# Kernel tuning notes

Hardware: AMD Instinct MI355X
Metric: run time of the kernel (lower is better)

Reference implementation:

```python
import jax, jax.numpy as jnp
import numpy as np

N, K, D_IN, D_OUT = 20000, 32, 128, 128


def _xavier(key, shape, gain):
    fan_out, fan_in = shape
    bound = gain * np.sqrt(6.0 / (fan_in + fan_out))
    return jax.random.uniform(key, shape, jnp.float32, -bound, bound)


def setup_inputs() -> dict:
    key = jax.random.key(0)
    ks = jax.random.split(key, 8)
    gain = np.sqrt(2.0)  # calculate_gain('relu')
    return {
        "data_x": jax.random.normal(ks[0], (N, D_IN), jnp.float32),
        "dists_max": jax.random.uniform(ks[1], (N, K), jnp.float32),
        "dists_argmax": jax.random.randint(ks[2], (N, K), 0, N, jnp.int64),
        # dist_compute: Nonlinear(1, D_OUT, 1)
        "w1d": _xavier(ks[3], (D_OUT, 1), gain),
        "b1d": jnp.zeros((D_OUT,), jnp.float32),
        "w2d": _xavier(ks[4], (1, D_OUT), gain),
        "b2d": jnp.zeros((1,), jnp.float32),
        # linear_hidden: (2*D_IN) -> D_OUT
        "wh": _xavier(ks[5], (D_OUT, 2 * D_IN), gain),
        "bh": jnp.zeros((D_OUT,), jnp.float32),
        # linear_out_position: D_OUT -> 1
        "wp": _xavier(ks[6], (1, D_OUT), gain),
        "bp": jnp.zeros((1,), jnp.float32),
    }


def reference(data_x, dists_max, dists_argmax, w1d, b1d, w2d, b2d, wh, bh, wp, bp):
    # trainable distance transform: [N,K] -> [N,K,1] -> MLP -> [N,K]
    d = jax.nn.relu(dists_max[..., None] * w1d[:, 0] + b1d)  # [N,K,D_OUT]
    d = (d @ w2d[0] + b2d[0])  # [N,K]
    # gather anchor features: [N,K,D_IN]
    subset = data_x[dists_argmax]
    messages = subset * d[..., None]
    self_feat = jnp.broadcast_to(data_x[:, None, :], messages.shape)
    cat = jnp.concatenate((messages, self_feat), axis=-1)  # [N,K,2*D_IN]
    h = jax.nn.relu(jnp.einsum('nkd,od->nko', cat, wh) + bh)  # [N,K,D_OUT]
    out_position = (h @ wp[0] + bp[0])  # [N,K]
    out_structure = jnp.mean(h, axis=1)  # [N,D_OUT]
    return out_position, out_structure
```

## Files before the change

kernel.cpp:

```cpp
#include <hip/hip_runtime.h>
#include <hip/hip_bf16.h>

#define N_ROWS 20000
#define KNN 32
#define DIN 128
#define DOUT 128

__global__ __launch_bounds__(256) void pack_wt(const float* __restrict__ wh,
                                               float* __restrict__ WTp) {
    int tid = blockIdx.x * 256 + threadIdx.x;
    int i  = tid & 3;
    int j  = (tid >> 2) & 255;
    int d4 = tid >> 10;
    int d  = d4 * 4 + i;
    float v = (j < 128) ? wh[j * 256 + d] : wh[(j - 128) * 256 + 128 + d];
    WTp[tid] = v;
}

__global__ __launch_bounds__(256) void gemm_xaxb(const float* __restrict__ x,
                                                 const float* __restrict__ WTp,
                                                 const float* __restrict__ bh,
                                                 __hip_bfloat16* __restrict__ XA16,
                                                 float* __restrict__ XBp) {
    __shared__ float xs[32][128];
    const int t = threadIdx.x;
    const int row0 = blockIdx.x * 32;

    #pragma unroll
    for (int i = 0; i < 4; ++i) {
        int idx = t + i * 256;
        int r = idx >> 5, c4 = idx & 31;
        ((float4*)xs[r])[c4] = ((const float4*)(x + (size_t)(row0 + r) * DIN))[c4];
    }
    __syncthreads();

    const int tx = t & 63;
    const int ty = t >> 6;
    const int r0 = ty * 8;
    float acc[8][4];
    #pragma unroll
    for (int r = 0; r < 8; ++r)
        #pragma unroll
        for (int c = 0; c < 4; ++c) acc[r][c] = 0.f;

    const float4* W4 = (const float4*)WTp;
    for (int d4 = 0; d4 < 32; ++d4) {
        float4 w0 = W4[d4 * 256 + tx];
        float4 w1 = W4[d4 * 256 + 64 + tx];
        float4 w2 = W4[d4 * 256 + 128 + tx];
        float4 w3 = W4[d4 * 256 + 192 + tx];
        #pragma unroll
        for (int r = 0; r < 8; ++r) {
            float4 xv = ((const float4*)xs[r0 + r])[d4];
            acc[r][0] += xv.x * w0.x + xv.y * w0.y + xv.z * w0.z + xv.w * w0.w;
            acc[r][1] += xv.x * w1.x + xv.y * w1.y + xv.z * w1.z + xv.w * w1.w;
            acc[r][2] += xv.x * w2.x + xv.y * w2.y + xv.z * w2.z + xv.w * w2.w;
            acc[r][3] += xv.x * w3.x + xv.y * w3.y + xv.z * w3.z + xv.w * w3.w;
        }
    }

    float bh0 = bh[tx], bh1 = bh[64 + tx];
    #pragma unroll
    for (int r = 0; r < 8; ++r) {
        size_t gr = row0 + r0 + r;
        XA16[gr * DOUT + tx]       = __float2bfloat16(acc[r][0]);
        XA16[gr * DOUT + 64 + tx]  = __float2bfloat16(acc[r][1]);
        XBp [gr * DOUT + tx]       = acc[r][2] + bh0;
        XBp [gr * DOUT + 64 + tx]  = acc[r][3] + bh1;
    }
}

__global__ __launch_bounds__(128) void fused_main(const float* __restrict__ dists,
                                                  const int*  __restrict__ argm,
                                                  const float* __restrict__ w1d,
                                                  const float* __restrict__ b1d,
                                                  const float* __restrict__ w2d,
                                                  const float* __restrict__ b2d,
                                                  const float* __restrict__ wp,
                                                  const float* __restrict__ bp,
                                                  const __hip_bfloat16* __restrict__ XA16,
                                                  const float* __restrict__ XBp,
                                                  float* __restrict__ out_pos,
                                                  float* __restrict__ out_struct) {
    const int w    = threadIdx.x >> 6;
    const int lane = threadIdx.x & 63;
    const int n    = blockIdx.x * 2 + w;

    __shared__ float pos_lds[2][KNN][65];
    __shared__ float d_lds[2][KNN];
    __shared__ int   idx_lds[2][KNN];

    {
        int k = lane >> 1, sub = lane & 1;
        float s = dists[(size_t)n * KNN + k];
        float a = 0.f;
        int ob = sub * 64;
        #pragma unroll
        for (int o4 = 0; o4 < 16; ++o4) {
            float4 w1 = ((const float4*)(w1d + ob))[o4];
            float4 b1 = ((const float4*)(b1d + ob))[o4];
            float4 w2 = ((const float4*)(w2d + ob))[o4];
            a += fmaxf(fmaf(s, w1.x, b1.x), 0.f) * w2.x;
            a += fmaxf(fmaf(s, w1.y, b1.y), 0.f) * w2.y;
            a += fmaxf(fmaf(s, w1.z, b1.z), 0.f) * w2.z;
            a += fmaxf(fmaf(s, w1.w, b1.w), 0.f) * w2.w;
        }
        a += __shfl_xor(a, 1);
        if (sub == 0) d_lds[w][k] = a + b2d[0];
        if (lane < KNN) idx_lds[w][lane] = argm[(size_t)n * KNN + lane];
    }

    float2 base = *(const float2*)(XBp + (size_t)n * DOUT + lane * 2);
    float2 wpv  = *(const float2*)(wp + lane * 2);
    __syncthreads();

    const unsigned short* xa_base = (const unsigned short*)XA16;
    float s0 = 0.f, s1 = 0.f;
    #pragma unroll
    for (int kk = 0; kk < KNN; ++kk) {
        float dk = d_lds[w][kk];
        int   m  = idx_lds[w][kk];
        unsigned u = *(const unsigned*)(xa_base + (size_t)m * DOUT + lane * 2);
        float xa0 = __uint_as_float(u << 16);
        float xa1 = __uint_as_float(u & 0xFFFF0000u);
        float h0 = fmaxf(fmaf(dk, xa0, base.x), 0.f);
        float h1 = fmaxf(fmaf(dk, xa1, base.y), 0.f);
        s0 += h0; s1 += h1;
        pos_lds[w][kk][lane] = fmaf(h1, wpv.y, h0 * wpv.x);
    }
    *(float2*)(out_struct + (size_t)n * DOUT + lane * 2) =
        make_float2(s0 * (1.f / KNN), s1 * (1.f / KNN));
    __syncthreads();

    {
        int k2 = lane & 31, half = lane >> 5;
        const float* row = &pos_lds[w][k2][half * 32];
        float p = 0.f;
        #pragma unroll
        for (int j = 0; j < 32; ++j) p += row[j];
        p += __shfl_xor(p, 32);
        if (lane < KNN)
            out_pos[(size_t)n * KNN + lane] = p + bp[0];
    }
}

extern "C" void kernel_launch(void* const* d_in, const int* in_sizes, int n_in,
                              void* d_out, int out_size, void* d_ws, size_t ws_size,
                              hipStream_t stream) {
    const float* data_x = (const float*)d_in[0];
    const float* dists  = (const float*)d_in[1];
    const int*   argm   = (const int*)d_in[2];
    const float* w1d    = (const float*)d_in[3];
    const float* b1d    = (const float*)d_in[4];
    const float* w2d    = (const float*)d_in[5];
    const float* b2d    = (const float*)d_in[6];
    const float* wh     = (const float*)d_in[7];
    const float* bh     = (const float*)d_in[8];
    const float* wp     = (const float*)d_in[9];
    const float* bp     = (const float*)d_in[10];

    float* out_pos    = (float*)d_out;
    float* out_struct = out_pos + (size_t)N_ROWS * KNN;

    float*          XBp  = (float*)d_ws;
    __hip_bfloat16* XA16 = (__hip_bfloat16*)(XBp + (size_t)N_ROWS * DOUT);
    float*          WTp  = (float*)((char*)XA16 + (size_t)N_ROWS * DOUT * 2);

    pack_wt<<<128, 256, 0, stream>>>(wh, WTp);
    gemm_xaxb<<<N_ROWS / 32, 256, 0, stream>>>(data_x, WTp, bh, XA16, XBp);
    fused_main<<<N_ROWS / 2, 128, 0, stream>>>(dists, argm, w1d, b1d, w2d, b2d,
                                               wp, bp, XA16, XBp, out_pos, out_struct);
}
```

Baseline: 170.5 us.

## Use one wave per row with readlane broadcasts and shuffle reductions

The fused kernel now runs one 64-thread wave per output row. The per-neighbour distance weights and indices stay in registers and are broadcast with readlane instead of being staged in LDS. The position dot product is partly reduced with lane shuffles, so only an 8-way partial sum per neighbour is written to a small LDS buffer instead of a full 32x65 array. Separately, the GEMM tile is halved to 16 rows per block to launch more blocks, at the cost of reusing each weight load across fewer rows.

After: 209.3 us. 1.23x slower.

```diff
diff --git a/kernel.cpp b/kernel.cpp
--- a/kernel.cpp
+++ b/kernel.cpp
@@ -22,12 +22,12 @@
                                                  const float* __restrict__ bh,
                                                  __hip_bfloat16* __restrict__ XA16,
                                                  float* __restrict__ XBp) {
-    __shared__ float xs[32][128];
+    __shared__ float xs[16][128];
     const int t = threadIdx.x;
-    const int row0 = blockIdx.x * 32;
+    const int row0 = blockIdx.x * 16;
 
     #pragma unroll
-    for (int i = 0; i < 4; ++i) {
+    for (int i = 0; i < 2; ++i) {
         int idx = t + i * 256;
         int r = idx >> 5, c4 = idx & 31;
         ((float4*)xs[r])[c4] = ((const float4*)(x + (size_t)(row0 + r) * DIN))[c4];
@@ -36,10 +36,10 @@
 
     const int tx = t & 63;
     const int ty = t >> 6;
-    const int r0 = ty * 8;
-    float acc[8][4];
+    const int r0 = ty * 4;
+    float acc[4][4];
     #pragma unroll
-    for (int r = 0; r < 8; ++r)
+    for (int r = 0; r < 4; ++r)
         #pragma unroll
         for (int c = 0; c < 4; ++c) acc[r][c] = 0.f;
 
@@ -50,7 +50,7 @@
         float4 w2 = W4[d4 * 256 + 128 + tx];
         float4 w3 = W4[d4 * 256 + 192 + tx];
         #pragma unroll
-        for (int r = 0; r < 8; ++r) {
+        for (int r = 0; r < 4; ++r) {
             float4 xv = ((const float4*)xs[r0 + r])[d4];
             acc[r][0] += xv.x * w0.x + xv.y * w0.y + xv.z * w0.z + xv.w * w0.w;
             acc[r][1] += xv.x * w1.x + xv.y * w1.y + xv.z * w1.z + xv.w * w1.w;
@@ -61,7 +61,7 @@
 
     float bh0 = bh[tx], bh1 = bh[64 + tx];
     #pragma unroll
-    for (int r = 0; r < 8; ++r) {
+    for (int r = 0; r < 4; ++r) {
         size_t gr = row0 + r0 + r;
         XA16[gr * DOUT + tx]       = __float2bfloat16(acc[r][0]);
         XA16[gr * DOUT + 64 + tx]  = __float2bfloat16(acc[r][1]);
@@ -70,77 +70,73 @@
     }
 }
 
-__global__ __launch_bounds__(128) void fused_main(const float* __restrict__ dists,
-                                                  const int*  __restrict__ argm,
-                                                  const float* __restrict__ w1d,
-                                                  const float* __restrict__ b1d,
-                                                  const float* __restrict__ w2d,
-                                                  const float* __restrict__ b2d,
-                                                  const float* __restrict__ wp,
-                                                  const float* __restrict__ bp,
-                                                  const __hip_bfloat16* __restrict__ XA16,
-                                                  const float* __restrict__ XBp,
-                                                  float* __restrict__ out_pos,
-                                                  float* __restrict__ out_struct) {
-    const int w    = threadIdx.x >> 6;
-    const int lane = threadIdx.x & 63;
-    const int n    = blockIdx.x * 2 + w;
+__global__ __launch_bounds__(64, 8) void fused_main(const float* __restrict__ dists,
+                                                    const int*  __restrict__ argm,
+                                                    const float* __restrict__ w1d,
+                                                    const float* __restrict__ b1d,
+                                                    const float* __restrict__ w2d,
+                                                    const float* __restrict__ b2d,
+                                                    const float* __restrict__ wp,
+                                                    const float* __restrict__ bp,
+                                                    const __hip_bfloat16* __restrict__ XA16,
+                                                    const float* __restrict__ XBp,
+                                                    float* __restrict__ out_pos,
+                                                    float* __restrict__ out_struct) {
+    const int n    = blockIdx.x;
+    const int lane = threadIdx.x;
 
-    __shared__ float pos_lds[2][KNN][65];
-    __shared__ float d_lds[2][KNN];
-    __shared__ int   idx_lds[2][KNN];
+    __shared__ float pos_p[KNN][9];
 
+    const int k = lane & 31, sub = lane >> 5;
+    float s = dists[(size_t)n * KNN + k];
+    float a = 0.f;
     {
-        int k = lane >> 1, sub = lane & 1;
-        float s = dists[(size_t)n * KNN + k];
-        float a = 0.f;
-        int ob = sub * 64;
+        const float4* W1 = (const float4*)(w1d + sub * 64);
+        const float4* B1 = (const float4*)(b1d + sub * 64);
+        const float4* W2 = (const float4*)(w2d + sub * 64);
         #pragma unroll
         for (int o4 = 0; o4 < 16; ++o4) {
-            float4 w1 = ((const float4*)(w1d + ob))[o4];
-            float4 b1 = ((const float4*)(b1d + ob))[o4];
-            float4 w2 = ((const float4*)(w2d + ob))[o4];
+            float4 w1 = W1[o4], b1 = B1[o4], w2 = W2[o4];
             a += fmaxf(fmaf(s, w1.x, b1.x), 0.f) * w2.x;
             a += fmaxf(fmaf(s, w1.y, b1.y), 0.f) * w2.y;
             a += fmaxf(fmaf(s, w1.z, b1.z), 0.f) * w2.z;
             a += fmaxf(fmaf(s, w1.w, b1.w), 0.f) * w2.w;
         }
-        a += __shfl_xor(a, 1);
-        if (sub == 0) d_lds[w][k] = a + b2d[0];
-        if (lane < KNN) idx_lds[w][lane] = argm[(size_t)n * KNN + lane];
     }
+    a += __shfl_xor(a, 32);
+    const float dval = a + b2d[0];
+    const int   idxv = argm[(size_t)n * KNN + k];
 
-    float2 base = *(const float2*)(XBp + (size_t)n * DOUT + lane * 2);
-    float2 wpv  = *(const float2*)(wp + lane * 2);
-    __syncthreads();
+    const float2 base = *(const float2*)(XBp + (size_t)n * DOUT + lane * 2);
+    const float2 wpv  = *(const float2*)(wp + lane * 2);
 
-    const unsigned short* xa_base = (const unsigned short*)XA16;
+    const unsigned* xa32 = (const unsigned*)XA16;
     float s0 = 0.f, s1 = 0.f;
     #pragma unroll
     for (int kk = 0; kk < KNN; ++kk) {
-        float dk = d_lds[w][kk];
-        int   m  = idx_lds[w][kk];
-        unsigned u = *(const unsigned*)(xa_base + (size_t)m * DOUT + lane * 2);
+        int   m  = __builtin_amdgcn_readlane(idxv, kk);
+        float dk = __int_as_float(__builtin_amdgcn_readlane(__float_as_int(dval), kk));
+        unsigned u = xa32[(size_t)m * 64 + lane];
         float xa0 = __uint_as_float(u << 16);
         float xa1 = __uint_as_float(u & 0xFFFF0000u);
         float h0 = fmaxf(fmaf(dk, xa0, base.x), 0.f);
         float h1 = fmaxf(fmaf(dk, xa1, base.y), 0.f);
         s0 += h0; s1 += h1;
-        pos_lds[w][kk][lane] = fmaf(h1, wpv.y, h0 * wpv.x);
+        float pv = fmaf(h1, wpv.y, h0 * wpv.x);
+        pv += __shfl_xor(pv, 1);
+        pv += __shfl_xor(pv, 2);
+        pv += __shfl_xor(pv, 4);
+        if ((lane & 7) == 0) pos_p[kk][lane >> 3] = pv;
     }
     *(float2*)(out_struct + (size_t)n * DOUT + lane * 2) =
         make_float2(s0 * (1.f / KNN), s1 * (1.f / KNN));
     __syncthreads();
 
-    {
-        int k2 = lane & 31, half = lane >> 5;
-        const float* row = &pos_lds[w][k2][half * 32];
-        float p = 0.f;
-        #pragma unroll
-        for (int j = 0; j < 32; ++j) p += row[j];
-        p += __shfl_xor(p, 32);
-        if (lane < KNN)
-            out_pos[(size_t)n * KNN + lane] = p + bp[0];
+    if (lane < KNN) {
+        const float* row = pos_p[lane];
+        float p = ((row[0] + row[1]) + (row[2] + row[3]))
+                + ((row[4] + row[5]) + (row[6] + row[7]));
+        out_pos[(size_t)n * KNN + lane] = p + bp[0];
     }
 }
 
@@ -167,7 +163,7 @@
     float*          WTp  = (float*)((char*)XA16 + (size_t)N_ROWS * DOUT * 2);
 
     pack_wt<<<128, 256, 0, stream>>>(wh, WTp);
-    gemm_xaxb<<<N_ROWS / 32, 256, 0, stream>>>(data_x, WTp, bh, XA16, XBp);
-    fused_main<<<N_ROWS / 2, 128, 0, stream>>>(dists, argm, w1d, b1d, w2d, b2d,
-                                               wp, bp, XA16, XBp, out_pos, out_struct);
+    gemm_xaxb<<<N_ROWS / 16, 256, 0, stream>>>(data_x, WTp, bh, XA16, XBp);
+    fused_main<<<N_ROWS, 64, 0, stream>>>(dists, argm, w1d, b1d, w2d, b2d,
+                                          wp, bp, XA16, XBp, out_pos, out_struct);
 }
```
